# Optimization experiments

Measured on AMD Instinct MI355X. Metric: run time of the kernel, lower is better.

The kernel has to match this reference:

```python
import jax, jax.numpy as jnp
import numpy as np

EPS = 1e-8
TAU = 1.0


def graph_conv(h_in, adj, W, b):
    # h: [N, D_out]
    h = h_in @ W
    nrm = jnp.linalg.norm(h, axis=1, keepdims=True)
    h_norm = h / jnp.maximum(nrm, EPS)  # F.normalize with eps clamp
    # cosine-sim logits + log-adjacency mask -> row softmax
    logits = (h_norm @ h_norm.T) / TAU + jnp.log(adj + EPS)  # [N, N]
    attn = jax.nn.softmax(logits, axis=1)
    return attn @ h + b


def setup_inputs() -> dict:
    key = jax.random.key(0)
    ks = jax.random.split(key, 20)
    N, F, H, C = 4096, 512, 128, 16

    def xavier(k, fan_in, fan_out):
        s = float(np.sqrt(6.0 / (fan_in + fan_out)))
        return jax.random.uniform(k, (fan_in, fan_out), minval=-s, maxval=s, dtype=jnp.float32)

    return {
        "x": jax.random.normal(ks[0], (N, F), dtype=jnp.float32),
        "adj_low": jax.random.uniform(ks[1], (N, N), dtype=jnp.float32),
        "adj_high": jax.random.uniform(ks[2], (N, N), dtype=jnp.float32),
        "adj_mid": jax.random.uniform(ks[3], (N, N), dtype=jnp.float32),
        "w_low0": xavier(ks[4], F, H), "b_low0": jnp.zeros((H,), jnp.float32),
        "w_high0": xavier(ks[5], F, H), "b_high0": jnp.zeros((H,), jnp.float32),
        "w_mid0": xavier(ks[6], F, H), "b_mid0": jnp.zeros((H,), jnp.float32),
        "w_low1": xavier(ks[7], H, C), "b_low1": jnp.zeros((C,), jnp.float32),
        "w_high1": xavier(ks[8], H, C), "b_high1": jnp.zeros((C,), jnp.float32),
        "w_mid1": xavier(ks[9], H, C), "b_mid1": jnp.zeros((C,), jnp.float32),
        "g0": jnp.ones((3,), jnp.float32),
        "g1": jnp.ones((3,), jnp.float32),
    }


def reference(x, adj_low, adj_high, adj_mid,
              w_low0, b_low0, w_high0, b_high0, w_mid0, b_mid0,
              w_low1, b_low1, w_high1, b_high1, w_mid1, b_mid1,
              g0, g1):
    # layer 0 (inner layer: ReLU; dropout p=0 in eval mode -> identity)
    hl = jax.nn.relu(graph_conv(x, adj_low, w_low0, b_low0))
    hh = jax.nn.relu(graph_conv(x, adj_high, w_high0, b_high0))
    hm = jax.nn.relu(graph_conv(x, adj_mid, w_mid0, b_mid0))
    w = jax.nn.softmax(g0)
    h = w[0] * hl + w[1] * hh + w[2] * hm

    # layer 1 (final layer: no activation)
    hl = graph_conv(h, adj_low, w_low1, b_low1)
    hh = graph_conv(h, adj_high, w_high1, b_high1)
    hm = graph_conv(h, adj_mid, w_mid1, b_mid1)
    w = jax.nn.softmax(g1)
    h = w[0] * hl + w[1] * hh + w[2] * hm

    return jax.nn.log_softmax(h, axis=-1)
```

## Files before the change

kernel.cpp:

```cpp
#include <hip/hip_runtime.h>

#define N_NODES 4096
#define F_IN 512
#define H_DIM 128
#define C_DIM 16
#define EPSF 1e-8f
#define LOG2E 1.4426950408889634f
#define SMAX 2.0f
#define NKS0 8
#define KLEN0 (N_NODES / NKS0)
#define NT0 (KLEN0 / 32)
#define NKS1 8

typedef __attribute__((ext_vector_type(8))) short bf16x8;
typedef __attribute__((ext_vector_type(4))) short bf16x4;
typedef __attribute__((ext_vector_type(4))) float f32x4;

__device__ __forceinline__ ushort f2bf(float f){
  union { float f; unsigned u; } v; v.f = f;
  unsigned u = v.u;
  return (ushort)((u + 0x7fffu + ((u >> 16) & 1u)) >> 16);
}
__device__ __forceinline__ float bf2f(ushort h){
  union { unsigned u; float f; } v; v.u = ((unsigned)h) << 16;
  return v.f;
}

__global__ __launch_bounds__(256) void proj0_kernel(
    const float* __restrict__ x,
    const float* __restrict__ Wl, const float* __restrict__ Wh,
    const float* __restrict__ Wm,
    ushort* __restrict__ hn, ushort* __restrict__ hvT)
{
  const int t = threadIdx.x;
  const int d = t & 127;
  const int half = t >> 7;
  const int r0 = blockIdx.x * 8;
  __shared__ float xs[8][F_IN];
  for (int i = t; i < 8 * F_IN; i += 256)
    xs[i >> 9][i & 511] = x[(size_t)(r0 + (i >> 9)) * F_IN + (i & 511)];
  __syncthreads();

  float acc0[8], acc1[8], acc2[8];
#pragma unroll
  for (int r = 0; r < 8; r++) { acc0[r] = 0.f; acc1[r] = 0.f; acc2[r] = 0.f; }

  const int k0 = half * (F_IN / 2);
  for (int k = k0; k < k0 + F_IN / 2; k++) {
    float wl = Wl[k * H_DIM + d];
    float wh = Wh[k * H_DIM + d];
    float wm = Wm[k * H_DIM + d];
#pragma unroll
    for (int r = 0; r < 8; r++) {
      float xv = xs[r][k];
      acc0[r] = fmaf(xv, wl, acc0[r]);
      acc1[r] = fmaf(xv, wh, acc1[r]);
      acc2[r] = fmaf(xv, wm, acc2[r]);
    }
  }

  __shared__ float part[3][8][128];
  if (half == 1) {
#pragma unroll
    for (int r = 0; r < 8; r++) {
      part[0][r][d] = acc0[r]; part[1][r][d] = acc1[r]; part[2][r][d] = acc2[r];
    }
  }
  __syncthreads();
  if (half == 0) {
#pragma unroll
    for (int r = 0; r < 8; r++) {
      acc0[r] += part[0][r][d]; acc1[r] += part[1][r][d]; acc2[r] += part[2][r][d];
    }
  }

  __shared__ float red[24][2];
  const int wv = t >> 6;
  const int lane = t & 63;

#define REDUCE_BRANCH(ACC, B)                                        \
  _Pragma("unroll")                                                  \
  for (int r = 0; r < 8; r++) {                                      \
    float v = ACC[r] * ACC[r];                                       \
    v += __shfl_down(v, 32); v += __shfl_down(v, 16);                \
    v += __shfl_down(v, 8);  v += __shfl_down(v, 4);                 \
    v += __shfl_down(v, 2);  v += __shfl_down(v, 1);                 \
    if (lane == 0) red[(B) * 8 + r][wv] = v;                         \
  }
  if (half == 0) {
    REDUCE_BRANCH(acc0, 0)
    REDUCE_BRANCH(acc1, 1)
    REDUCE_BRANCH(acc2, 2)
  }
  __syncthreads();

#define WRITE_BRANCH(ACC, B)                                                   \
  _Pragma("unroll")                                                            \
  for (int r = 0; r < 8; r++) {                                                \
    float nrm = sqrtf(red[(B) * 8 + r][0] + red[(B) * 8 + r][1]);              \
    float rn = 1.0f / fmaxf(nrm, EPSF);                                        \
    float h = ACC[r];                                                          \
    hn[((size_t)(B) * N_NODES + r0 + r) * H_DIM + d] = f2bf(h * rn);           \
    hvT[((size_t)(B) * H_DIM + d) * N_NODES + r0 + r] = f2bf(h);               \
  }
  if (half == 0) {
    WRITE_BRANCH(acc0, 0)
    WRITE_BRANCH(acc1, 1)
    WRITE_BRANCH(acc2, 2)
  }
#undef REDUCE_BRANCH
#undef WRITE_BRANCH
}

__global__ __launch_bounds__(256) void flash0_kernel(
    const ushort* __restrict__ hn, const ushort* __restrict__ hvT,
    const float* __restrict__ adj_l, const float* __restrict__ adj_h,
    const float* __restrict__ adj_m,
    float* __restrict__ pl0, ushort* __restrict__ pO)
{
  const int tid = threadIdx.x;
  const int w = tid >> 6;
  const int lane = tid & 63;
  const int lr = lane & 15;
  const int lg = lane >> 4;
  const int ks = blockIdx.y;
  const int b = blockIdx.z;
  const int qblk = blockIdx.x * 64;
  const int q0 = qblk + w * 16;
  const float* adj = (b == 0) ? adj_l : (b == 1) ? adj_h : adj_m;
  const ushort* Qg = hn + (size_t)b * N_NODES * H_DIM;
  const ushort* VTg = hvT + (size_t)b * H_DIM * N_NODES;
  const int kbase = ks * KLEN0;

  __shared__ ushort sK[2][32 * 128];
  __shared__ ushort sV[2][128 * 32];
  __shared__ float  sAdj[2][64 * 32];

  bf16x8 qf[4];
  {
    const ushort* qp = Qg + (size_t)(q0 + lr) * H_DIM + lg * 8;
#pragma unroll
    for (int u = 0; u < 4; u++) qf[u] = *(const bf16x8*)(qp + 32 * u);
  }

  f32x4 o[8];
#pragma unroll
  for (int dt = 0; dt < 8; dt++) o[dt] = (f32x4){0.f, 0.f, 0.f, 0.f};
  float lsum = 0.f;

  const int sA = w * 128 + lane;
  const int sB = sA + 64;
  const int kkA = sA >> 4, kcA = sA & 15;
  const int kkB = sB >> 4, kcB = sB & 15;
  const size_t kOffA = (size_t)kkA * H_DIM + ((size_t)(kcA ^ (kkA & 7)) << 3);
  const size_t kOffB = (size_t)kkB * H_DIM + ((size_t)(kcB ^ (kkB & 7)) << 3);
  const int dA = sA >> 2, vcA = sA & 3;
  const int dB = sB >> 2, vcB = sB & 3;
  const size_t vOffA = (size_t)dA * N_NODES + ((size_t)(vcA ^ ((dA >> 1) & 3)) << 3);
  const size_t vOffB = (size_t)dB * N_NODES + ((size_t)(vcB ^ ((dB >> 1) & 3)) << 3);
  const int arw1 = tid >> 3, ac1 = tid & 7;
  const int arw2 = arw1 + 32;
  const size_t aOff1 = (size_t)arw1 * N_NODES + ((size_t)(ac1 ^ (arw1 & 7)) << 2);
  const size_t aOff2 = (size_t)arw2 * N_NODES + ((size_t)(ac1 ^ (arw2 & 7)) << 2);
  const float* adjq = adj + (size_t)qblk * N_NODES;

#define STAGE(BUF, K0)                                                         \
  {                                                                            \
    const ushort* ksrc = Qg + (size_t)(K0) * H_DIM;                            \
    const ushort* vsrc = VTg + (K0);                                           \
    const float*  asrc = adjq + (K0);                                          \
    __builtin_amdgcn_global_load_lds(ksrc + kOffA,                             \
        (char*)&sK[BUF][0] + w * 2048, 16, 0, 0);                              \
    __builtin_amdgcn_global_load_lds(ksrc + kOffB,                             \
        (char*)&sK[BUF][0] + w * 2048 + 1024, 16, 0, 0);                       \
    __builtin_amdgcn_global_load_lds(vsrc + vOffA,                             \
        (char*)&sV[BUF][0] + w * 2048, 16, 0, 0);                              \
    __builtin_amdgcn_global_load_lds(vsrc + vOffB,                             \
        (char*)&sV[BUF][0] + w * 2048 + 1024, 16, 0, 0);                       \
    __builtin_amdgcn_global_load_lds(asrc + aOff1,                             \
        (char*)&sAdj[BUF][0] + w * 1024, 16, 0, 0);                            \
    __builtin_amdgcn_global_load_lds(asrc + aOff2,                             \
        (char*)&sAdj[BUF][0] + 4096 + w * 1024, 16, 0, 0);                     \
  }

  STAGE(0, kbase)

  const int rL = w * 16 + lr;
  const int adr0 = rL * 32 + ((lg ^ (rL & 7)) << 2);
  const int adr1 = rL * 32 + (((4 + lg) ^ (rL & 7)) << 2);

  for (int t = 0; t < NT0; t++) {
    const int cur = t & 1;
    __builtin_amdgcn_s_barrier();
    __builtin_amdgcn_sched_barrier(0);
    if (t + 1 < NT0) STAGE(cur ^ 1, kbase + (t + 1) * 32)
    if (t + 1 < NT0) { asm volatile("s_waitcnt vmcnt(6)" ::: "memory"); }
    else             { asm volatile("s_waitcnt vmcnt(0)" ::: "memory"); }
    __builtin_amdgcn_sched_barrier(0);
    __builtin_amdgcn_s_barrier();
    __builtin_amdgcn_sched_barrier(0);

    __builtin_amdgcn_s_setprio(1);
    f32x4 s0 = (f32x4){0.f, 0.f, 0.f, 0.f};
    f32x4 s1 = (f32x4){0.f, 0.f, 0.f, 0.f};
    const char* sKc = (const char*)&sK[cur][0];
#pragma unroll
    for (int u = 0; u < 4; u++) {
      const int c0 = lg + 4 * u;
      bf16x8 kf0 = *(const bf16x8*)(sKc + lr * 256 + ((c0 ^ (lr & 7)) << 4));
      bf16x8 kf1 = *(const bf16x8*)(sKc + (lr + 16) * 256 + ((c0 ^ (lr & 7)) << 4));
      s0 = __builtin_amdgcn_mfma_f32_16x16x32_bf16(kf0, qf[u], s0, 0, 0, 0);
      s1 = __builtin_amdgcn_mfma_f32_16x16x32_bf16(kf1, qf[u], s1, 0, 0, 0);
    }
    f32x4 a0 = *(const f32x4*)&sAdj[cur][adr0];
    f32x4 a1 = *(const f32x4*)&sAdj[cur][adr1];
    bf16x4 pf0, pf1;
#pragma unroll
    for (int r = 0; r < 4; r++) {
      float p0 = exp2f(fmaf(s0[r], LOG2E, -SMAX)) * (a0[r] + EPSF);
      float p1 = exp2f(fmaf(s1[r], LOG2E, -SMAX)) * (a1[r] + EPSF);
      lsum += p0 + p1;
      pf0[r] = (short)f2bf(p0);
      pf1[r] = (short)f2bf(p1);
    }
    const char* sVc = (const char*)&sV[cur][0];
#pragma unroll
    for (int dt = 0; dt < 8; dt++) {
      const int dd = dt * 16 + lr;
      const int sw = (dd >> 1) & 3;
      bf16x4 vf0 = *(const bf16x4*)(sVc + dd * 64 +
                     ((((lg >> 1) + 0) ^ sw) << 4) + (lg & 1) * 8);
      bf16x4 vf1 = *(const bf16x4*)(sVc + dd * 64 +
                     ((((lg >> 1) + 2) ^ sw) << 4) + (lg & 1) * 8);
      o[dt] = __builtin_amdgcn_mfma_f32_16x16x16bf16_1k(pf0, vf0, o[dt], 0, 0, 0);
      o[dt] = __builtin_amdgcn_mfma_f32_16x16x16bf16_1k(pf1, vf1, o[dt], 0, 0, 0);
    }
    __builtin_amdgcn_s_setprio(0);
  }
#undef STAGE

  const int ps = b * NKS0 + ks;
  float psum = lsum;
  psum += __shfl_xor(psum, 16);
  psum += __shfl_xor(psum, 32);
  if (lg == 0) pl0[(size_t)ps * N_NODES + q0 + lr] = psum;
#pragma unroll
  for (int dt = 0; dt < 8; dt++) {
#pragma unroll
    for (int r = 0; r < 4; r++) {
      pO[((size_t)ps * N_NODES + q0 + lg * 4 + r) * H_DIM + dt * 16 + lr] =
          f2bf(o[dt][r]);
    }
  }
}

__global__ __launch_bounds__(128) void mix1_kernel(
    const float* __restrict__ pl0, const ushort* __restrict__ pO,
    const float* __restrict__ bl0, const float* __restrict__ bh0,
    const float* __restrict__ bm0,
    const float* __restrict__ Wl1, const float* __restrict__ Wh1,
    const float* __restrict__ Wm1,
    const float* __restrict__ g0,
    ushort* __restrict__ hn1b, ushort* __restrict__ hbT)
{
  const int q = blockIdx.x;
  const int t = threadIdx.x;
  float ga = g0[0], gb = g0[1], gc = g0[2];
  float gm = fmaxf(ga, fmaxf(gb, gc));
  float e0 = expf(ga - gm), e1 = expf(gb - gm), e2 = expf(gc - gm);
  float ei = 1.0f / (e0 + e1 + e2);

  __shared__ float Ls[3];
  if (t < 3) {
    float L = 0.f;
#pragma unroll
    for (int ks = 0; ks < NKS0; ks++) L += pl0[(size_t)(t * NKS0 + ks) * N_NODES + q];
    Ls[t] = L;
  }
  float O0 = 0.f, O1 = 0.f, O2 = 0.f;
#pragma unroll
  for (int ks = 0; ks < NKS0; ks++) {
    O0 += bf2f(pO[((size_t)(0 * NKS0 + ks) * N_NODES + q) * H_DIM + t]);
    O1 += bf2f(pO[((size_t)(1 * NKS0 + ks) * N_NODES + q) * H_DIM + t]);
    O2 += bf2f(pO[((size_t)(2 * NKS0 + ks) * N_NODES + q) * H_DIM + t]);
  }
  __syncthreads();

  __shared__ float hc[H_DIM];
  hc[t] = e0 * ei * fmaxf(O0 / Ls[0] + bl0[t], 0.f)
        + e1 * ei * fmaxf(O1 / Ls[1] + bh0[t], 0.f)
        + e2 * ei * fmaxf(O2 / Ls[2] + bm0[t], 0.f);
  __syncthreads();

  __shared__ float shb[48];
  if (t < 48) {
    const int b = t >> 4, j = t & 15;
    const float* W = (b == 0) ? Wl1 : (b == 1) ? Wh1 : Wm1;
    float s = 0.f;
    for (int k = 0; k < H_DIM; k++) s = fmaf(hc[k], W[k * C_DIM + j], s);
    shb[t] = s;
  }
  __syncthreads();
  __shared__ float rns[3];
  if (t < 3) {
    float s = 0.f;
#pragma unroll
    for (int j = 0; j < C_DIM; j++) { float u = shb[t * C_DIM + j]; s = fmaf(u, u, s); }
    rns[t] = 1.0f / fmaxf(sqrtf(s), EPSF);
  }
  __syncthreads();
  if (t < 48) {
    const int b = t >> 4, j = t & 15;
    hbT[((size_t)b * C_DIM + j) * N_NODES + q] = f2bf(shb[t]);
    hn1b[((size_t)b * N_NODES + q) * C_DIM + j] = f2bf(shb[t] * rns[b]);
  }
}

__global__ __launch_bounds__(256) void flash1_kernel(
    const ushort* __restrict__ hn1b, const ushort* __restrict__ hbT,
    const float* __restrict__ adj_l, const float* __restrict__ adj_h,
    const float* __restrict__ adj_m,
    float* __restrict__ pl, float* __restrict__ pacc)
{
  const int tid = threadIdx.x;
  const int wid = tid >> 6;
  const int lane = tid & 63;
  const int lr = lane & 15;
  const int lg = lane >> 4;
  const int qblk = blockIdx.x * 64;
  const int q0 = qblk + wid * 16;
  const int ks = blockIdx.y;
  const int b = blockIdx.z;
  const float* adj = (b == 0) ? adj_l : (b == 1) ? adj_h : adj_m;
  const ushort* Qn = hn1b + (size_t)b * N_NODES * C_DIM;
  const ushort* VT = hbT + (size_t)b * C_DIM * N_NODES;
  const int kbase = ks * (N_NODES / NKS1);
  const int nt = (N_NODES / NKS1) / 32;

  __shared__ float sAdj[2][64 * 32];

  const bf16x4 qf = *(const bf16x4*)(Qn + (size_t)(q0 + lr) * C_DIM + lg * 4);
  const f32x4 zero = (f32x4){0.f, 0.f, 0.f, 0.f};
  f32x4 o = zero;
  float lsum = 0.f;
  const ushort* vrow = VT + (size_t)lr * N_NODES;

  const int rowA = tid >> 3, cA = tid & 7;
  const int rowB = rowA + 32;
  const size_t aOffA = (size_t)rowA * N_NODES + ((size_t)(cA ^ (rowA & 7)) << 2);
  const size_t aOffB = (size_t)rowB * N_NODES + ((size_t)(cA ^ (rowB & 7)) << 2);
  const float* adjq = adj + (size_t)qblk * N_NODES;

#define STAGE1(BUF, K0)                                                        \
  {                                                                            \
    const float* asrc = adjq + (K0);                                           \
    __builtin_amdgcn_global_load_lds(asrc + aOffA,                             \
        (char*)&sAdj[BUF][0] + wid * 1024, 16, 0, 0);                          \
    __builtin_amdgcn_global_load_lds(asrc + aOffB,                             \
        (char*)&sAdj[BUF][0] + 4096 + wid * 1024, 16, 0, 0);                   \
  }

  STAGE1(0, kbase)

  const int rowL = wid * 16 + lr;
  const int adr0 = rowL * 32 + ((lg ^ (rowL & 7)) << 2);
  const int adr1 = rowL * 32 + (((4 + lg) ^ (rowL & 7)) << 2);

  for (int t = 0; t < nt; t++) {
    const int cur = t & 1;
    __syncthreads();
    if (t + 1 < nt) STAGE1(cur ^ 1, kbase + (t + 1) * 32)

    const int k0 = kbase + t * 32;
    bf16x4 kf0 = *(const bf16x4*)(Qn + (size_t)(k0 + lr) * C_DIM + lg * 4);
    bf16x4 kf1 = *(const bf16x4*)(Qn + (size_t)(k0 + 16 + lr) * C_DIM + lg * 4);
    f32x4 s0 = __builtin_amdgcn_mfma_f32_16x16x16bf16_1k(kf0, qf, zero, 0, 0, 0);
    f32x4 s1 = __builtin_amdgcn_mfma_f32_16x16x16bf16_1k(kf1, qf, zero, 0, 0, 0);
    f32x4 a0 = *(const f32x4*)&sAdj[cur][adr0];
    f32x4 a1 = *(const f32x4*)&sAdj[cur][adr1];
    bf16x4 pf0, pf1;
#pragma unroll
    for (int r = 0; r < 4; r++) {
      float e0 = exp2f(fmaf(s0[r], LOG2E, -SMAX));
      float e1 = exp2f(fmaf(s1[r], LOG2E, -SMAX));
      float p0 = e0 * (a0[r] + EPSF);
      float p1 = e1 * (a1[r] + EPSF);
      lsum += p0 + p1;
      pf0[r] = (short)f2bf(p0);
      pf1[r] = (short)f2bf(p1);
    }
    bf16x4 vf0 = *(const bf16x4*)(vrow + k0 + lg * 4);
    bf16x4 vf1 = *(const bf16x4*)(vrow + k0 + 16 + lg * 4);
    o = __builtin_amdgcn_mfma_f32_16x16x16bf16_1k(pf0, vf0, o, 0, 0, 0);
    o = __builtin_amdgcn_mfma_f32_16x16x16bf16_1k(pf1, vf1, o, 0, 0, 0);
  }
#undef STAGE1

  const int ps = b * NKS1 + ks;
  float psum = lsum;
  psum += __shfl_xor(psum, 16);
  psum += __shfl_xor(psum, 32);
  if (lg == 0) pl[(size_t)ps * N_NODES + q0 + lr] = psum;
#pragma unroll
  for (int r = 0; r < 4; r++)
    pacc[((size_t)ps * N_NODES + q0 + lg * 4 + r) * C_DIM + lr] = o[r];
}

__global__ __launch_bounds__(256) void combine1_kernel(
    const float* __restrict__ pl, const float* __restrict__ pacc,
    float* __restrict__ o1)
{
  const int q = blockIdx.x * 256 + threadIdx.x;
  const int b = blockIdx.y;
  float L = 0.f;
  f32x4 out0 = (f32x4){0,0,0,0}, out1 = (f32x4){0,0,0,0},
        out2 = (f32x4){0,0,0,0}, out3 = (f32x4){0,0,0,0};
#pragma unroll
  for (int ks = 0; ks < NKS1; ks++) {
    const size_t pidx = (size_t)(b * NKS1 + ks) * N_NODES + q;
    L += pl[pidx];
    const f32x4* pa = (const f32x4*)(pacc + pidx * C_DIM);
    out0 += pa[0]; out1 += pa[1]; out2 += pa[2]; out3 += pa[3];
  }
  float invL = 1.0f / L;
  f32x4* dst = (f32x4*)(o1 + ((size_t)b * N_NODES + q) * C_DIM);
  dst[0] = out0 * invL; dst[1] = out1 * invL; dst[2] = out2 * invL; dst[3] = out3 * invL;
}

__global__ __launch_bounds__(256) void final_kernel(
    const float* __restrict__ o1,
    const float* __restrict__ bl1, const float* __restrict__ bh1,
    const float* __restrict__ bm1,
    const float* __restrict__ g1, float* __restrict__ out)
{
  const int q = blockIdx.x * 256 + threadIdx.x;
  float ga = g1[0], gb = g1[1], gc = g1[2];
  float gm = fmaxf(ga, fmaxf(gb, gc));
  float e0 = expf(ga - gm), e1 = expf(gb - gm), e2 = expf(gc - gm);
  float ei = 1.0f / (e0 + e1 + e2);
  float w0 = e0 * ei, w1 = e1 * ei, w2 = e2 * ei;
  const size_t NC = (size_t)N_NODES * C_DIM;

  float v[16];
#pragma unroll
  for (int i = 0; i < 4; i++) {
    f32x4 a = ((const f32x4*)(o1 + (size_t)q * C_DIM))[i];
    f32x4 bA = ((const f32x4*)(o1 + NC + (size_t)q * C_DIM))[i];
    f32x4 c = ((const f32x4*)(o1 + 2 * NC + (size_t)q * C_DIM))[i];
    f32x4 xl = ((const f32x4*)bl1)[i];
    f32x4 xh = ((const f32x4*)bh1)[i];
    f32x4 xm = ((const f32x4*)bm1)[i];
#pragma unroll
    for (int j = 0; j < 4; j++)
      v[i * 4 + j] = w0 * (a[j] + xl[j]) + w1 * (bA[j] + xh[j]) + w2 * (c[j] + xm[j]);
  }
  float mx = -1e30f;
#pragma unroll
  for (int j = 0; j < 16; j++) mx = fmaxf(mx, v[j]);
  float se = 0.f;
#pragma unroll
  for (int j = 0; j < 16; j++) se += expf(v[j] - mx);
  float lse = mx + logf(se);
  f32x4* dst = (f32x4*)(out + (size_t)q * C_DIM);
#pragma unroll
  for (int i = 0; i < 4; i++) {
    f32x4 r;
#pragma unroll
    for (int j = 0; j < 4; j++) r[j] = v[i * 4 + j] - lse;
    dst[i] = r;
  }
}

extern "C" void kernel_launch(void* const* d_in, const int* in_sizes, int n_in,
                              void* d_out, int out_size, void* d_ws, size_t ws_size,
                              hipStream_t stream) {
  (void)in_sizes; (void)n_in; (void)out_size; (void)ws_size;
  const float* x     = (const float*)d_in[0];
  const float* adj_l = (const float*)d_in[1];
  const float* adj_h = (const float*)d_in[2];
  const float* adj_m = (const float*)d_in[3];
  const float* w_l0  = (const float*)d_in[4];
  const float* b_l0  = (const float*)d_in[5];
  const float* w_h0  = (const float*)d_in[6];
  const float* b_h0  = (const float*)d_in[7];
  const float* w_m0  = (const float*)d_in[8];
  const float* b_m0  = (const float*)d_in[9];
  const float* w_l1  = (const float*)d_in[10];
  const float* b_l1  = (const float*)d_in[11];
  const float* w_h1  = (const float*)d_in[12];
  const float* b_h1  = (const float*)d_in[13];
  const float* w_m1  = (const float*)d_in[14];
  const float* b_m1  = (const float*)d_in[15];
  const float* g0    = (const float*)d_in[16];
  const float* g1    = (const float*)d_in[17];
  float* out = (float*)d_out;

  char* ws = (char*)d_ws;
  ushort* hn  = (ushort*)(ws);
  ushort* hvT = (ushort*)(ws + (3u << 20));
  ushort* hn1b= (ushort*)(ws + (6u << 20));
  ushort* hbT = (ushort*)(ws + (6u << 20) + (384u << 10));
  float*  pl0 = (float*)(ws + (12u << 20));
  ushort* pO  = (ushort*)(ws + (12u << 20) + (512u << 10));
  float*  pl  = (float*)(ws + (12u << 20));
  float*  pacc= (float*)(ws + (13u << 20));
  float*  o1  = (float*)(ws + (20u << 20));

  proj0_kernel<<<dim3(512), dim3(256), 0, stream>>>(x, w_l0, w_h0, w_m0, hn, hvT);
  flash0_kernel<<<dim3(64, NKS0, 3), dim3(256), 0, stream>>>(hn, hvT, adj_l, adj_h, adj_m,
                                                             pl0, pO);
  mix1_kernel<<<dim3(4096), dim3(128), 0, stream>>>(pl0, pO, b_l0, b_h0, b_m0,
                                                    w_l1, w_h1, w_m1, g0, hn1b, hbT);
  flash1_kernel<<<dim3(64, NKS1, 3), dim3(256), 0, stream>>>(hn1b, hbT, adj_l, adj_h, adj_m,
                                                             pl, pacc);
  combine1_kernel<<<dim3(16, 3), dim3(256), 0, stream>>>(pl, pacc, o1);
  final_kernel<<<dim3(16), dim3(256), 0, stream>>>(o1, b_l1, b_h1, b_m1, g1, out);
}
```

Before: 162.2 us.

## Halve layer-0 key splits and stage adjacency in 64-column groups

Layer-0 attention now splits the key range into 4 chunks instead of 8, so each block runs twice as many tiles and writes fewer partial outputs. The adjacency tile is loaded in 64-column groups (256 B rows) once every two iterations, with its own double buffer and a new vmcnt accounting scheme. The aim is wider, more coalesced adjacency reads and less partial-reduction traffic. The cost is more LDS per block, half as many blocks for occupancy, and a more fragile wait-count schedule; the mix kernel must also agree with the new NKS0.

Result: slower. 184.3 us (+13.6%).

```diff
diff --git a/kernel.cpp b/kernel.cpp
--- a/kernel.cpp
+++ b/kernel.cpp
@@ -7,9 +7,10 @@
 #define EPSF 1e-8f
 #define LOG2E 1.4426950408889634f
 #define SMAX 2.0f
-#define NKS0 8
+#define NKS0 4
 #define KLEN0 (N_NODES / NKS0)
 #define NT0 (KLEN0 / 32)
+#define NGRP0 (NT0 / 2)
 #define NKS1 8
 
 typedef __attribute__((ext_vector_type(8))) short bf16x8;
@@ -134,7 +135,7 @@
 
   __shared__ ushort sK[2][32 * 128];
   __shared__ ushort sV[2][128 * 32];
-  __shared__ float  sAdj[2][64 * 32];
+  __shared__ float  sAdj[2][64 * 64];
 
   bf16x8 qf[4];
   {
@@ -158,17 +159,19 @@
   const int dB = sB >> 2, vcB = sB & 3;
   const size_t vOffA = (size_t)dA * N_NODES + ((size_t)(vcA ^ ((dA >> 1) & 3)) << 3);
   const size_t vOffB = (size_t)dB * N_NODES + ((size_t)(vcB ^ ((dB >> 1) & 3)) << 3);
-  const int arw1 = tid >> 3, ac1 = tid & 7;
-  const int arw2 = arw1 + 32;
-  const size_t aOff1 = (size_t)arw1 * N_NODES + ((size_t)(ac1 ^ (arw1 & 7)) << 2);
-  const size_t aOff2 = (size_t)arw2 * N_NODES + ((size_t)(ac1 ^ (arw2 & 7)) << 2);
+  size_t aOffJ[4];
+#pragma unroll
+  for (int j = 0; j < 4; j++) {
+    const int u = w * 64 + lane + j * 256;
+    const int r = u >> 4, c = u & 15;
+    aOffJ[j] = (size_t)r * N_NODES + ((size_t)(c ^ (r & 7)) << 2);
+  }
   const float* adjq = adj + (size_t)qblk * N_NODES;
 
-#define STAGE(BUF, K0)                                                         \
+#define STAGE_KV(BUF, K0)                                                      \
   {                                                                            \
     const ushort* ksrc = Qg + (size_t)(K0) * H_DIM;                            \
     const ushort* vsrc = VTg + (K0);                                           \
-    const float*  asrc = adjq + (K0);                                          \
     __builtin_amdgcn_global_load_lds(ksrc + kOffA,                             \
         (char*)&sK[BUF][0] + w * 2048, 16, 0, 0);                              \
     __builtin_amdgcn_global_load_lds(ksrc + kOffB,                             \
@@ -177,25 +180,37 @@
         (char*)&sV[BUF][0] + w * 2048, 16, 0, 0);                              \
     __builtin_amdgcn_global_load_lds(vsrc + vOffB,                             \
         (char*)&sV[BUF][0] + w * 2048 + 1024, 16, 0, 0);                       \
-    __builtin_amdgcn_global_load_lds(asrc + aOff1,                             \
-        (char*)&sAdj[BUF][0] + w * 1024, 16, 0, 0);                            \
-    __builtin_amdgcn_global_load_lds(asrc + aOff2,                             \
-        (char*)&sAdj[BUF][0] + 4096 + w * 1024, 16, 0, 0);                     \
-  }
-
-  STAGE(0, kbase)
+  }
+#define STAGE_ADJ(BUF, K0)                                                     \
+  {                                                                            \
+    const float* asrc = adjq + (K0);                                           \
+    __builtin_amdgcn_global_load_lds(asrc + aOffJ[0],                          \
+        (char*)&sAdj[BUF][0] + (w * 64 + 0) * 16, 16, 0, 0);                   \
+    __builtin_amdgcn_global_load_lds(asrc + aOffJ[1],                          \
+        (char*)&sAdj[BUF][0] + (w * 64 + 256) * 16, 16, 0, 0);                 \
+    __builtin_amdgcn_global_load_lds(asrc + aOffJ[2],                          \
+        (char*)&sAdj[BUF][0] + (w * 64 + 512) * 16, 16, 0, 0);                 \
+    __builtin_amdgcn_global_load_lds(asrc + aOffJ[3],                          \
+        (char*)&sAdj[BUF][0] + (w * 64 + 768) * 16, 16, 0, 0);                 \
+  }
+
+  STAGE_ADJ(0, kbase)
+  STAGE_KV(0, kbase)
 
   const int rL = w * 16 + lr;
-  const int adr0 = rL * 32 + ((lg ^ (rL & 7)) << 2);
-  const int adr1 = rL * 32 + (((4 + lg) ^ (rL & 7)) << 2);
 
   for (int t = 0; t < NT0; t++) {
     const int cur = t & 1;
+    const int gb = (t >> 1) & 1;
     __builtin_amdgcn_s_barrier();
     __builtin_amdgcn_sched_barrier(0);
-    if (t + 1 < NT0) STAGE(cur ^ 1, kbase + (t + 1) * 32)
-    if (t + 1 < NT0) { asm volatile("s_waitcnt vmcnt(6)" ::: "memory"); }
-    else             { asm volatile("s_waitcnt vmcnt(0)" ::: "memory"); }
+    if (t + 1 < NT0) STAGE_KV(cur ^ 1, kbase + (t + 1) * 32)
+    if ((t & 1) == 0 && (t >> 1) + 1 < NGRP0)
+      STAGE_ADJ(gb ^ 1, kbase + ((t >> 1) + 1) * 64)
+    const int rem = NT0 - 1 - t;
+    if (rem >= 2)      { asm volatile("s_waitcnt vmcnt(8)" ::: "memory"); }
+    else if (rem == 1) { asm volatile("s_waitcnt vmcnt(4)" ::: "memory"); }
+    else               { asm volatile("s_waitcnt vmcnt(0)" ::: "memory"); }
     __builtin_amdgcn_sched_barrier(0);
     __builtin_amdgcn_s_barrier();
     __builtin_amdgcn_sched_barrier(0);
@@ -212,8 +227,12 @@
       s0 = __builtin_amdgcn_mfma_f32_16x16x32_bf16(kf0, qf[u], s0, 0, 0, 0);
       s1 = __builtin_amdgcn_mfma_f32_16x16x32_bf16(kf1, qf[u], s1, 0, 0, 0);
     }
-    f32x4 a0 = *(const f32x4*)&sAdj[cur][adr0];
-    f32x4 a1 = *(const f32x4*)&sAdj[cur][adr1];
+    const int lc0 = (t & 1) * 8 + lg;
+    const int lc1 = lc0 + 4;
+    f32x4 a0 = *(const f32x4*)((const char*)&sAdj[gb][0] +
+                   rL * 256 + ((lc0 ^ (rL & 7)) << 4));
+    f32x4 a1 = *(const f32x4*)((const char*)&sAdj[gb][0] +
+                   rL * 256 + ((lc1 ^ (rL & 7)) << 4));
     bf16x4 pf0, pf1;
 #pragma unroll
     for (int r = 0; r < 4; r++) {
@@ -237,7 +256,8 @@
     }
     __builtin_amdgcn_s_setprio(0);
   }
-#undef STAGE
+#undef STAGE_KV
+#undef STAGE_ADJ
 
   const int ps = b * NKS0 + ks;
   float psum = lsum;
```
